# Performance work log

Measured on AMD Instinct MI355X. Metric: run time of the kernel, lower is better.

Reference implementation:

```python
import jax, jax.numpy as jnp
import numpy as np

D = 768
HEAD_SIZE = 64  # D // 12


def setup_inputs() -> dict:
    key = jax.random.key(0)
    k_ix, k_wk, k_wq, k_wv = jax.random.split(key, 4)
    ix = jax.random.normal(k_ix, (4, 4096, D), dtype=jnp.float32)
    s = 1.0 / np.sqrt(D)
    Wk = jax.random.normal(k_wk, (D, HEAD_SIZE), dtype=jnp.float32) * s
    Wq = jax.random.normal(k_wq, (D, HEAD_SIZE), dtype=jnp.float32) * s
    Wv = jax.random.normal(k_wv, (D, HEAD_SIZE), dtype=jnp.float32) * s
    return {"ix": ix, "Wk": Wk, "Wq": Wq, "Wv": Wv}


def reference(ix, Wk, Wq, Wv):
    # ix: [B, N, D]; W*: [D, h]
    k = ix @ Wk            # [B, N, h]
    q = ix @ Wq            # [B, N, h]
    v = ix @ Wv            # [B, N, h]
    scale = HEAD_SIZE ** -0.5
    wei = jnp.einsum('bnh,bmh->bnm', q, k) * scale  # [B, N, N]
    wei = jax.nn.softmax(wei, axis=-1)
    out = jnp.einsum('bnm,bmh->bnh', wei, v)        # [B, N, h]
    return out
```

## Files before the change

### kernel.cpp

```cpp
#include <hip/hip_runtime.h>
#include <math.h>

#define Dm   768
#define Hm   64
#define SEQ  4096
#define NB   4
#define NROW (NB * SEQ)

#define QSCALE (0.125f * 1.4426950408889634f)

typedef _Float16 f16;
typedef __attribute__((ext_vector_type(8))) _Float16 f16x8;
typedef __attribute__((ext_vector_type(2))) __fp16 fp16x2_raw;
typedef __attribute__((ext_vector_type(4))) float f32x4;
typedef unsigned int uint;
typedef unsigned short ushort;

#define MFMAH(A, B, C) __builtin_amdgcn_mfma_f32_16x16x32_f16(A, B, C, 0, 0, 0)

__device__ __forceinline__ uint pkrtz(float a, float b) {
    fp16x2_raw r = __builtin_amdgcn_cvt_pkrtz(a, b);
    return __builtin_bit_cast(uint, r);
}
__device__ __forceinline__ ushort f2h(float f) {
    f16 h = (f16)f;
    return __builtin_bit_cast(ushort, h);
}
union F16x8U { uint u[4]; f16x8 v; };

__global__ __launch_bounds__(256) void wconv(
    const float* __restrict__ Wq, const float* __restrict__ Wk,
    const float* __restrict__ Wv, ushort* __restrict__ WTt)
{
    const int c   = blockIdx.x;
    const int mat = c >> 6, col = c & 63;
    const float* W = (mat == 0) ? Wq : (mat == 1 ? Wk : Wv);
    const float sc = (mat == 0) ? QSCALE : 1.0f;
    for (int k = threadIdx.x; k < Dm; k += 256)
        WTt[((size_t)(k >> 5) * 192 + c) * 32 + (k & 31)] = f2h(W[k * 64 + col] * sc);
}

__global__ __launch_bounds__(256, 3) void proj(
    const float* __restrict__ ix, const ushort* __restrict__ WTt,
    ushort* __restrict__ Qw, ushort* __restrict__ Kt, ushort* __restrict__ Vt)
{
    __shared__ __align__(16) float comb[2][3072];

    const int t    = threadIdx.x;
    const int lane = t & 63;
    const int kh   = __builtin_amdgcn_readfirstlane(t >> 6);
    const int q15  = lane & 15, quad = lane >> 4;
    const int gr0  = blockIdx.x * 16;

    const float*  Ab = ix + (size_t)(gr0 + q15) * Dm + kh * 192 + quad * 8;
    const ushort* Bb = WTt + ((size_t)(kh * 6) * 192 + q15) * 32 + quad * 8;

    f32x4 acc[12];
#pragma unroll
    for (int ct = 0; ct < 12; ++ct) acc[ct] = (f32x4){0.f, 0.f, 0.f, 0.f};

    f32x4 Af[3][2];
#pragma unroll
    for (int i = 0; i < 2; ++i) {
        Af[i][0] = *(const f32x4*)(Ab + i * 32);
        Af[i][1] = *(const f32x4*)(Ab + i * 32 + 4);
    }

#pragma unroll
    for (int it = 0; it < 6; ++it) {
        f16x8 Bf[12];
#pragma unroll
        for (int ct = 0; ct < 12; ++ct)
            Bf[ct] = *(const f16x8*)(Bb + (size_t)it * 6144 + ct * 512);

        if (it + 2 < 6) {
            Af[(it + 2) % 3][0] = *(const f32x4*)(Ab + (it + 2) * 32);
            Af[(it + 2) % 3][1] = *(const f32x4*)(Ab + (it + 2) * 32 + 4);
        }

        F16x8U af;
        af.u[0] = pkrtz(Af[it % 3][0].x, Af[it % 3][0].y);
        af.u[1] = pkrtz(Af[it % 3][0].z, Af[it % 3][0].w);
        af.u[2] = pkrtz(Af[it % 3][1].x, Af[it % 3][1].y);
        af.u[3] = pkrtz(Af[it % 3][1].z, Af[it % 3][1].w);
#pragma unroll
        for (int ct = 0; ct < 12; ++ct)
            acc[ct] = MFMAH(af.v, Bf[ct], acc[ct]);
    }

    if (kh >= 2) {
#pragma unroll
        for (int ct = 0; ct < 12; ++ct)
            *(f32x4*)&comb[kh - 2][(ct * 64 + lane) * 4] = acc[ct];
    }
    __syncthreads();
    if (kh < 2) {
#pragma unroll
        for (int ct = 0; ct < 12; ++ct) {
            f32x4 o = *(const f32x4*)&comb[kh][(ct * 64 + lane) * 4];
            acc[ct].x += o.x; acc[ct].y += o.y; acc[ct].z += o.z; acc[ct].w += o.w;
        }
    }
    __syncthreads();
    if (kh == 1) {
#pragma unroll
        for (int ct = 0; ct < 12; ++ct)
            *(f32x4*)&comb[0][(ct * 64 + lane) * 4] = acc[ct];
    }
    __syncthreads();
    if (kh == 0) {
#pragma unroll
        for (int ct = 0; ct < 12; ++ct) {
            f32x4 o = *(const f32x4*)&comb[0][(ct * 64 + lane) * 4];
            acc[ct].x += o.x; acc[ct].y += o.y; acc[ct].z += o.z; acc[ct].w += o.w;
        }
        const int h16 = (gr0 >> 4) & 1;
        const int n4  = gr0 >> 4;
        const int j32 = gr0 >> 5;
#pragma unroll
        for (int ct = 0; ct < 12; ++ct) {
            float vals[4] = {acc[ct].x, acc[ct].y, acc[ct].z, acc[ct].w};
            if (ct < 4) {
#pragma unroll
                for (int r = 0; r < 4; ++r)
                    Qw[(size_t)(gr0 + quad * 4 + r) * 64 + ct * 16 + q15] = f2h(vals[r]);
            } else if (ct < 8) {
#pragma unroll
                for (int r = 0; r < 4; ++r)
                    Kt[(size_t)n4 * 1024 + (ct - 4) * 256 + (quad * 4 + r) * 16 + q15] = f2h(vals[r]);
            } else {
                ushort4 vv;
                vv.x = f2h(vals[0]); vv.y = f2h(vals[1]);
                vv.z = f2h(vals[2]); vv.w = f2h(vals[3]);
                *(ushort4*)(Vt + (size_t)j32 * 2048 + (ct - 8) * 512 +
                            (h16 * 2 + (quad >> 1)) * 128 + q15 * 8 + (quad & 1) * 4) = vv;
            }
        }
    }
}

__global__ __launch_bounds__(512, 2) void attn(
    const ushort* __restrict__ Qw, const ushort* __restrict__ Kt,
    const ushort* __restrict__ Vt, float* __restrict__ out)
{
    __shared__ __align__(16) float aF[20992];
    short* aS = (short*)aF;

    const int t    = threadIdx.x;
    const int lane = t & 63;
    const int w    = __builtin_amdgcn_readfirstlane(t >> 6);
    const int q15  = lane & 15, quad = lane >> 4;

    const int bb    = blockIdx.x;
    const int xcd   = bb & 7;
    const int batch = xcd >> 1;
    const int slot  = (bb >> 3) | ((xcd & 1) << 5);
    const int q0    = slot * 64;
    const size_t base = (size_t)batch * SEQ;

    f16x8 qf[4][2];
#pragma unroll
    for (int g = 0; g < 4; ++g)
#pragma unroll
        for (int h = 0; h < 2; ++h)
            qf[g][h] = *(const f16x8*)(Qw + (base + q0 + g * 16 + q15) * 64 + h * 32 + quad * 8);

    f32x4 oacc[4][4];
#pragma unroll
    for (int g = 0; g < 4; ++g)
#pragma unroll
        for (int dt = 0; dt < 4; ++dt) oacc[g][dt] = (f32x4){0.f, 0.f, 0.f, 0.f};
    float lsum[4] = {0.f, 0.f, 0.f, 0.f};

    const size_t j0g = base + w * 512;
    const ushort* Kfb = Kt + (j0g >> 4) * 1024;
    const ushort* Vfb = Vt + (j0g >> 5) * 2048 + lane * 8;
    short* Ps = aS + w * 5120;

    int koff[2][2];
#pragma unroll
    for (int jt = 0; jt < 2; ++jt)
#pragma unroll
        for (int h = 0; h < 2; ++h)
            koff[jt][h] = jt * 1024 + h * 512 + (quad >> 1) * 256 + q15 * 16 + (quad & 1) * 8;

    f16x8 kf[3][2][2], vf[3][4];

#define LOADKV(slotc, i)                                                       \
    {                                                                          \
        _Pragma("unroll") for (int jt = 0; jt < 2; ++jt)                       \
        _Pragma("unroll") for (int h = 0; h < 2; ++h)                          \
            kf[slotc][jt][h] = *(const f16x8*)(Kfb + (size_t)(i) * 2048 + koff[jt][h]); \
        _Pragma("unroll") for (int dt = 0; dt < 4; ++dt)                       \
            vf[slotc][dt] = *(const f16x8*)(Vfb + (size_t)(i) * 2048 + dt * 512); \
    }
#define QKSTEP(slotc, pb)                                                      \
    {                                                                          \
        _Pragma("unroll") for (int g = 0; g < 4; ++g)                          \
        _Pragma("unroll") for (int jt = 0; jt < 2; ++jt) {                     \
            f32x4 z = (f32x4){0.f, 0.f, 0.f, 0.f};                             \
            z = MFMAH(kf[slotc][jt][0], qf[g][0], z);                          \
            z = MFMAH(kf[slotc][jt][1], qf[g][1], z);                          \
            float e0 = exp2f(z.x), e1 = exp2f(z.y);                            \
            float e2 = exp2f(z.z), e3 = exp2f(z.w);                            \
            lsum[g] += (e0 + e1) + (e2 + e3);                                  \
            uint2 pk = make_uint2(pkrtz(e0, e1), pkrtz(e2, e3));               \
            *(uint2*)(Ps + (pb) * 2560 + (g * 16 + q15) * 40 + jt * 16 + quad * 4) = pk; \
        }                                                                      \
    }
#define PVSTEP(slotc, pb)                                                      \
    {                                                                          \
        f16x8 pf[4];                                                           \
        _Pragma("unroll") for (int g = 0; g < 4; ++g)                          \
            pf[g] = *(const f16x8*)(Ps + (pb) * 2560 + (g * 16 + q15) * 40 + quad * 8); \
        _Pragma("unroll") for (int dt = 0; dt < 4; ++dt)                       \
        _Pragma("unroll") for (int g = 0; g < 4; ++g)                          \
            oacc[g][dt] = MFMAH(pf[g], vf[slotc][dt], oacc[g][dt]);            \
    }

    LOADKV(0, 0);
    LOADKV(1, 1);
    QKSTEP(0, 0);
#pragma unroll
    for (int i = 0; i < 16; ++i) {
        if (i + 2 < 16) LOADKV((i + 2) % 3, i + 2);
        if (i + 1 < 16) QKSTEP((i + 1) % 3, (i + 1) & 1);
        PVSTEP(i % 3, i & 1);
    }

#pragma unroll
    for (int g = 0; g < 4; ++g) {
        lsum[g] += __shfl_xor(lsum[g], 16);
        lsum[g] += __shfl_xor(lsum[g], 32);
    }
    if (quad == 0) {
#pragma unroll
        for (int g = 0; g < 4; ++g)
            aF[20480 + w * 64 + g * 16 + q15] = lsum[g];
    }
    __syncthreads();

#define OWRITE(idx)                                                          \
    {                                                                        \
        float* b = aF + (idx) * 4096;                                        \
        _Pragma("unroll") for (int g = 0; g < 4; ++g)                        \
        _Pragma("unroll") for (int dt = 0; dt < 4; ++dt) {                   \
            b[(g * 16 + quad * 4 + 0) * 64 + dt * 16 + q15] = oacc[g][dt].x; \
            b[(g * 16 + quad * 4 + 1) * 64 + dt * 16 + q15] = oacc[g][dt].y; \
            b[(g * 16 + quad * 4 + 2) * 64 + dt * 16 + q15] = oacc[g][dt].z; \
            b[(g * 16 + quad * 4 + 3) * 64 + dt * 16 + q15] = oacc[g][dt].w; \
        }                                                                    \
    }
#define OADD(idx)                                                            \
    {                                                                        \
        const float* b = aF + (idx) * 4096;                                  \
        _Pragma("unroll") for (int g = 0; g < 4; ++g)                        \
        _Pragma("unroll") for (int dt = 0; dt < 4; ++dt) {                   \
            oacc[g][dt].x += b[(g * 16 + quad * 4 + 0) * 64 + dt * 16 + q15];\
            oacc[g][dt].y += b[(g * 16 + quad * 4 + 1) * 64 + dt * 16 + q15];\
            oacc[g][dt].z += b[(g * 16 + quad * 4 + 2) * 64 + dt * 16 + q15];\
            oacc[g][dt].w += b[(g * 16 + quad * 4 + 3) * 64 + dt * 16 + q15];\
        }                                                                    \
    }
    if (w >= 4) OWRITE(w - 4);
    __syncthreads();
    if (w < 4) OADD(w);
    __syncthreads();
    if (w == 2 || w == 3) OWRITE(w - 2);
    __syncthreads();
    if (w < 2) OADD(w);
    __syncthreads();
    if (w < 2) OWRITE(w);
    __syncthreads();

    {
        const int q  = t >> 3;
        const int d0 = (t & 7) * 8;
        float l = 0.f;
#pragma unroll
        for (int i = 0; i < 8; ++i) l += aF[20480 + i * 64 + q];
        const float linv = 1.0f / l;
#pragma unroll
        for (int k2 = 0; k2 < 2; ++k2) {
            float4 a = *(const float4*)&aF[q * 64 + d0 + k2 * 4];
            float4 b = *(const float4*)&aF[4096 + q * 64 + d0 + k2 * 4];
            float4 s;
            s.x = (a.x + b.x) * linv; s.y = (a.y + b.y) * linv;
            s.z = (a.z + b.z) * linv; s.w = (a.w + b.w) * linv;
            *(float4*)(out + (base + q0 + q) * 64 + d0 + k2 * 4) = s;
        }
    }
}

extern "C" void kernel_launch(void* const* d_in, const int* in_sizes, int n_in,
                              void* d_out, int out_size, void* d_ws, size_t ws_size,
                              hipStream_t stream)
{
    const float* ix = (const float*)d_in[0];
    const float* Wk = (const float*)d_in[1];
    const float* Wq = (const float*)d_in[2];
    const float* Wv = (const float*)d_in[3];
    float* out = (float*)d_out;

    ushort* Qw  = (ushort*)d_ws;
    ushort* Kt  = Qw + (size_t)NROW * Hm;
    ushort* Vt  = Kt + (size_t)NROW * Hm;
    ushort* WTt = Vt + (size_t)NROW * Hm;

    wconv<<<192, 256, 0, stream>>>(Wq, Wk, Wv, WTt);
    proj<<<1024, 256, 0, stream>>>(ix, WTt, Qw, Kt, Vt);
    attn<<<256, 512, 0, stream>>>(Qw, Kt, Vt, out);
}
```

Baseline: 135.5 us.

## Split attention keys across blocks with smaller tiles and a separate fixup reduction

The attention kernel now uses 256-thread blocks over 32 query rows, and each block covers only half of the key sequence. Grid size grows from 256 to 1024 blocks, which should fill the GPU better. Per-block partial outputs and row sums go to a global workspace, and a new fixup kernel adds the two halves and normalises. V is double-buffered instead of triple-buffered, which lowers register pressure. The cost is an extra kernel launch plus a global round trip for the partials, and each block reuses its K/V loads across fewer query rows.

```diff
diff --git a/kernel.cpp b/kernel.cpp
--- a/kernel.cpp
+++ b/kernel.cpp
@@ -139,11 +139,11 @@
     }
 }
 
-__global__ __launch_bounds__(512, 2) void attn(
+__global__ __launch_bounds__(256, 3) void attn_p1(
     const ushort* __restrict__ Qw, const ushort* __restrict__ Kt,
-    const ushort* __restrict__ Vt, float* __restrict__ out)
-{
-    __shared__ __align__(16) float aF[20992];
+    const ushort* __restrict__ Vt, float* __restrict__ po, float* __restrict__ pl)
+{
+    __shared__ __align__(16) float aF[5248];
     short* aS = (short*)aF;
 
     const int t    = threadIdx.x;
@@ -154,28 +154,29 @@
     const int bb    = blockIdx.x;
     const int xcd   = bb & 7;
     const int batch = xcd >> 1;
-    const int slot  = (bb >> 3) | ((xcd & 1) << 5);
-    const int q0    = slot * 64;
+    const int half  = xcd & 1;
+    const int slot  = bb >> 3;
+    const int q0    = slot * 32;
     const size_t base = (size_t)batch * SEQ;
 
-    f16x8 qf[4][2];
-#pragma unroll
-    for (int g = 0; g < 4; ++g)
+    f16x8 qf[2][2];
+#pragma unroll
+    for (int g = 0; g < 2; ++g)
 #pragma unroll
         for (int h = 0; h < 2; ++h)
             qf[g][h] = *(const f16x8*)(Qw + (base + q0 + g * 16 + q15) * 64 + h * 32 + quad * 8);
 
-    f32x4 oacc[4][4];
-#pragma unroll
-    for (int g = 0; g < 4; ++g)
+    f32x4 oacc[2][4];
+#pragma unroll
+    for (int g = 0; g < 2; ++g)
 #pragma unroll
         for (int dt = 0; dt < 4; ++dt) oacc[g][dt] = (f32x4){0.f, 0.f, 0.f, 0.f};
-    float lsum[4] = {0.f, 0.f, 0.f, 0.f};
-
-    const size_t j0g = base + w * 512;
+    float lsum[2] = {0.f, 0.f};
+
+    const size_t j0g = base + half * 2048 + w * 512;
     const ushort* Kfb = Kt + (j0g >> 4) * 1024;
     const ushort* Vfb = Vt + (j0g >> 5) * 2048 + lane * 8;
-    short* Ps = aS + w * 5120;
+    short* Ps = aS + w * 2560;
 
     int koff[2][2];
 #pragma unroll
@@ -184,66 +185,72 @@
         for (int h = 0; h < 2; ++h)
             koff[jt][h] = jt * 1024 + h * 512 + (quad >> 1) * 256 + q15 * 16 + (quad & 1) * 8;
 
-    f16x8 kf[3][2][2], vf[3][4];
-
-#define LOADKV(slotc, i)                                                       \
+    f16x8 kf[3][2][2];
+    f16x8 vf[2][4];
+
+#define LOADK(s, i)                                                            \
     {                                                                          \
         _Pragma("unroll") for (int jt = 0; jt < 2; ++jt)                       \
         _Pragma("unroll") for (int h = 0; h < 2; ++h)                          \
-            kf[slotc][jt][h] = *(const f16x8*)(Kfb + (size_t)(i) * 2048 + koff[jt][h]); \
+            kf[s][jt][h] = *(const f16x8*)(Kfb + (size_t)(i) * 2048 + koff[jt][h]); \
+    }
+#define LOADV(s, i)                                                            \
+    {                                                                          \
         _Pragma("unroll") for (int dt = 0; dt < 4; ++dt)                       \
-            vf[slotc][dt] = *(const f16x8*)(Vfb + (size_t)(i) * 2048 + dt * 512); \
-    }
-#define QKSTEP(slotc, pb)                                                      \
+            vf[s][dt] = *(const f16x8*)(Vfb + (size_t)(i) * 2048 + dt * 512);  \
+    }
+#define QKSTEP(s, pb)                                                          \
     {                                                                          \
-        _Pragma("unroll") for (int g = 0; g < 4; ++g)                          \
+        _Pragma("unroll") for (int g = 0; g < 2; ++g)                          \
         _Pragma("unroll") for (int jt = 0; jt < 2; ++jt) {                     \
             f32x4 z = (f32x4){0.f, 0.f, 0.f, 0.f};                             \
-            z = MFMAH(kf[slotc][jt][0], qf[g][0], z);                          \
-            z = MFMAH(kf[slotc][jt][1], qf[g][1], z);                          \
+            z = MFMAH(kf[s][jt][0], qf[g][0], z);                              \
+            z = MFMAH(kf[s][jt][1], qf[g][1], z);                              \
             float e0 = exp2f(z.x), e1 = exp2f(z.y);                            \
             float e2 = exp2f(z.z), e3 = exp2f(z.w);                            \
             lsum[g] += (e0 + e1) + (e2 + e3);                                  \
             uint2 pk = make_uint2(pkrtz(e0, e1), pkrtz(e2, e3));               \
-            *(uint2*)(Ps + (pb) * 2560 + (g * 16 + q15) * 40 + jt * 16 + quad * 4) = pk; \
+            *(uint2*)(Ps + (pb) * 1280 + (g * 16 + q15) * 40 + jt * 16 + quad * 4) = pk; \
         }                                                                      \
     }
-#define PVSTEP(slotc, pb)                                                      \
+#define PVSTEP(s, pb)                                                          \
     {                                                                          \
-        f16x8 pf[4];                                                           \
-        _Pragma("unroll") for (int g = 0; g < 4; ++g)                          \
-            pf[g] = *(const f16x8*)(Ps + (pb) * 2560 + (g * 16 + q15) * 40 + quad * 8); \
+        f16x8 pf[2];                                                           \
+        _Pragma("unroll") for (int g = 0; g < 2; ++g)                          \
+            pf[g] = *(const f16x8*)(Ps + (pb) * 1280 + (g * 16 + q15) * 40 + quad * 8); \
         _Pragma("unroll") for (int dt = 0; dt < 4; ++dt)                       \
-        _Pragma("unroll") for (int g = 0; g < 4; ++g)                          \
-            oacc[g][dt] = MFMAH(pf[g], vf[slotc][dt], oacc[g][dt]);            \
-    }
-
-    LOADKV(0, 0);
-    LOADKV(1, 1);
+        _Pragma("unroll") for (int g = 0; g < 2; ++g)                          \
+            oacc[g][dt] = MFMAH(pf[g], vf[s][dt], oacc[g][dt]);                \
+    }
+
+    LOADK(0, 0);
+    LOADV(0, 0);
+    LOADK(1, 1);
     QKSTEP(0, 0);
 #pragma unroll
     for (int i = 0; i < 16; ++i) {
-        if (i + 2 < 16) LOADKV((i + 2) % 3, i + 2);
+        if (i + 2 < 16) LOADK((i + 2) % 3, i + 2);
+        if (i + 1 < 16) LOADV((i + 1) & 1, i + 1);
         if (i + 1 < 16) QKSTEP((i + 1) % 3, (i + 1) & 1);
-        PVSTEP(i % 3, i & 1);
-    }
-
-#pragma unroll
-    for (int g = 0; g < 4; ++g) {
+        PVSTEP(i & 1, i & 1);
+    }
+
+#pragma unroll
+    for (int g = 0; g < 2; ++g) {
         lsum[g] += __shfl_xor(lsum[g], 16);
         lsum[g] += __shfl_xor(lsum[g], 32);
     }
     if (quad == 0) {
 #pragma unroll
-        for (int g = 0; g < 4; ++g)
-            aF[20480 + w * 64 + g * 16 + q15] = lsum[g];
+        for (int g = 0; g < 2; ++g)
+            aF[5120 + w * 32 + g * 16 + q15] = lsum[g];
     }
     __syncthreads();
 
 #define OWRITE(idx)                                                          \
     {                                                                        \
-        float* b = aF + (idx) * 4096;                                        \
-        _Pragma("unroll") for (int g = 0; g < 4; ++g)                        \
+        float* b = aF + (idx) * 2048;                                        \
+        _Pragma("unroll") for (int g = 0; g < 2; ++g)                        \
         _Pragma("unroll") for (int dt = 0; dt < 4; ++dt) {                   \
             b[(g * 16 + quad * 4 + 0) * 64 + dt * 16 + q15] = oacc[g][dt].x; \
             b[(g * 16 + quad * 4 + 1) * 64 + dt * 16 + q15] = oacc[g][dt].y; \
@@ -253,8 +260,8 @@
     }
 #define OADD(idx)                                                            \
     {                                                                        \
-        const float* b = aF + (idx) * 4096;                                  \
-        _Pragma("unroll") for (int g = 0; g < 4; ++g)                        \
+        const float* b = aF + (idx) * 2048;                                  \
+        _Pragma("unroll") for (int g = 0; g < 2; ++g)                        \
         _Pragma("unroll") for (int dt = 0; dt < 4; ++dt) {                   \
             oacc[g][dt].x += b[(g * 16 + quad * 4 + 0) * 64 + dt * 16 + q15];\
             oacc[g][dt].y += b[(g * 16 + quad * 4 + 1) * 64 + dt * 16 + q15];\
@@ -262,33 +269,60 @@
             oacc[g][dt].w += b[(g * 16 + quad * 4 + 3) * 64 + dt * 16 + q15];\
         }                                                                    \
     }
-    if (w >= 4) OWRITE(w - 4);
-    __syncthreads();
-    if (w < 4) OADD(w);
-    __syncthreads();
-    if (w == 2 || w == 3) OWRITE(w - 2);
+    if (w >= 2) OWRITE(w - 2);
     __syncthreads();
     if (w < 2) OADD(w);
     __syncthreads();
-    if (w < 2) OWRITE(w);
-    __syncthreads();
-
-    {
-        const int q  = t >> 3;
-        const int d0 = (t & 7) * 8;
-        float l = 0.f;
-#pragma unroll
-        for (int i = 0; i < 8; ++i) l += aF[20480 + i * 64 + q];
-        const float linv = 1.0f / l;
-#pragma unroll
-        for (int k2 = 0; k2 < 2; ++k2) {
-            float4 a = *(const float4*)&aF[q * 64 + d0 + k2 * 4];
-            float4 b = *(const float4*)&aF[4096 + q * 64 + d0 + k2 * 4];
-            float4 s;
-            s.x = (a.x + b.x) * linv; s.y = (a.y + b.y) * linv;
-            s.z = (a.z + b.z) * linv; s.w = (a.w + b.w) * linv;
-            *(float4*)(out + (base + q0 + q) * 64 + d0 + k2 * 4) = s;
-        }
+    if (w == 1) OWRITE(0);
+    __syncthreads();
+    if (w == 0) {
+        OADD(0);
+        float* pob = po + (size_t)bb * 2048;
+#pragma unroll
+        for (int g = 0; g < 2; ++g)
+#pragma unroll
+            for (int dt = 0; dt < 4; ++dt) {
+                pob[(g * 16 + quad * 4 + 0) * 64 + dt * 16 + q15] = oacc[g][dt].x;
+                pob[(g * 16 + quad * 4 + 1) * 64 + dt * 16 + q15] = oacc[g][dt].y;
+                pob[(g * 16 + quad * 4 + 2) * 64 + dt * 16 + q15] = oacc[g][dt].z;
+                pob[(g * 16 + quad * 4 + 3) * 64 + dt * 16 + q15] = oacc[g][dt].w;
+            }
+        if (quad == 0) {
+#pragma unroll
+            for (int g = 0; g < 2; ++g) {
+                int qq = g * 16 + q15;
+                float lt = aF[5120 + qq] + aF[5120 + 32 + qq] +
+                           aF[5120 + 64 + qq] + aF[5120 + 96 + qq];
+                pl[(size_t)bb * 32 + qq] = lt;
+            }
+        }
+    }
+}
+
+__global__ __launch_bounds__(256) void fixup(
+    const float* __restrict__ po, const float* __restrict__ pl,
+    float* __restrict__ out)
+{
+    const int g  = blockIdx.x * 256 + threadIdx.x;
+    const int n  = g >> 3;
+    const int d0 = (g & 7) * 8;
+    const int batch = n >> 12;
+    const int slot  = (n & 4095) >> 5;
+    const int q     = n & 31;
+    const int bb0 = (slot << 3) | (batch << 1);
+    const int bb1 = bb0 | 1;
+
+    const float linv = 1.0f / (pl[(size_t)bb0 * 32 + q] + pl[(size_t)bb1 * 32 + q]);
+    const float* p0 = po + (size_t)bb0 * 2048 + q * 64 + d0;
+    const float* p1 = po + (size_t)bb1 * 2048 + q * 64 + d0;
+#pragma unroll
+    for (int k2 = 0; k2 < 2; ++k2) {
+        float4 a = *(const float4*)(p0 + k2 * 4);
+        float4 b = *(const float4*)(p1 + k2 * 4);
+        float4 s;
+        s.x = (a.x + b.x) * linv; s.y = (a.y + b.y) * linv;
+        s.z = (a.z + b.z) * linv; s.w = (a.w + b.w) * linv;
+        *(float4*)(out + (size_t)n * 64 + d0 + k2 * 4) = s;
     }
 }
 
@@ -306,8 +340,11 @@
     ushort* Kt  = Qw + (size_t)NROW * Hm;
     ushort* Vt  = Kt + (size_t)NROW * Hm;
     ushort* WTt = Vt + (size_t)NROW * Hm;
+    float*  po  = (float*)(WTt + (size_t)24 * 192 * 32);
+    float*  pl  = po + (size_t)1024 * 2048;
 
     wconv<<<192, 256, 0, stream>>>(Wq, Wk, Wv, WTt);
     proj<<<1024, 256, 0, stream>>>(ix, WTt, Qw, Kt, Vt);
-    attn<<<256, 512, 0, stream>>>(Qw, Kt, Vt, out);
-}
+    attn_p1<<<1024, 256, 0, stream>>>(Qw, Kt, Vt, po, pl);
+    fixup<<<512, 256, 0, stream>>>(po, pl, out);
+}
```

Result: slower. 139.8 us (+3.2%).
